# Kernel tuning notes

Measured on AMD Instinct MI355X. Metric: run time of the kernel, lower is better.

The kernel has to match this reference:

```python
import jax, jax.numpy as jnp
import numpy as np

B, S, H, E, TOPK = 4, 2048, 2048, 8, 2


def setup_inputs() -> dict:
    key = jax.random.key(0)
    ks = jax.random.split(key, 3)
    scale_g = 1.0 / np.sqrt(H)
    scale_e = 1.0 / np.sqrt(H)
    return {
        "x": jax.random.normal(ks[0], (B, S, H), dtype=jnp.float32),
        "Wg": jax.random.normal(ks[1], (H, E), dtype=jnp.float32) * scale_g,
        "bg": jnp.zeros((E,), dtype=jnp.float32),
        "We": jax.random.normal(ks[2], (E, H, H), dtype=jnp.float32) * scale_e,
        "be": jnp.zeros((E, H), dtype=jnp.float32),
        "top_k": TOPK,
    }


def reference(x, Wg, bg, We, be, top_k):
    # x: [B, S, H]
    b, s, h = x.shape
    e = Wg.shape[1]
    tok = x.reshape(-1, h)                      # [T, H]
    logits = tok @ Wg + bg                      # [T, E]
    scores = jax.nn.softmax(logits, axis=-1)    # [T, E]
    _, idx = jax.lax.top_k(scores, top_k)       # [T, top_k]
    # per-expert membership mask: token routed to expert iff expert in its top-k
    mask = (idx[:, :, None] == jnp.arange(e)[None, None, :]).any(axis=1)  # [T, E]
    out = jnp.zeros_like(tok)
    for eid in range(e):  # small fixed expert loop (structurally distinct weights)
        gate = jnp.where(mask[:, eid], scores[:, eid], 0.0)  # [T]
        # dense per-expert layer; tokens not routed contribute exactly zero,
        # matching the torch gather -> dense -> scatter-add combine
        out = out + gate[:, None] * (tok @ We[eid] + be[eid])
    return out.reshape(b, s, h)
```

## Files before the change

### kernel.cpp

```cpp
#include <hip/hip_runtime.h>
#include <hip/hip_bf16.h>

#define TOK 8192
#define HD 2048
#define NE 8
#define KTOP 2
#define NSLOT (TOK * KTOP)
#define NCHUNK (TOK / 256)

typedef __attribute__((ext_vector_type(8))) short bf16x8;
typedef __attribute__((ext_vector_type(4))) float f32x4;

#define GLDS16(g, l) __builtin_amdgcn_global_load_lds( \
    (const __attribute__((address_space(1))) void*)(g), \
    (__attribute__((address_space(3))) void*)(l), 16, 0, 0)

__device__ __forceinline__ unsigned short f2bf(float f) {
  union { float f; unsigned u; } v; v.f = f;
  unsigned r = v.u + 0x7fffu + ((v.u >> 16) & 1u);
  return (unsigned short)(r >> 16);
}
__device__ __forceinline__ float bf2f(unsigned short b) {
  union { unsigned u; float f; } v; v.u = ((unsigned)b) << 16;
  return v.f;
}

__global__ __launch_bounds__(256) void routex_kernel(
    const float* __restrict__ x, const float* __restrict__ Wg, const float* __restrict__ bg,
    int* __restrict__ eidx2, float* __restrict__ gate2,
    unsigned short* __restrict__ xbf) {
  __shared__ float xs[HD];
  __shared__ float red[4][NE];
  int t = blockIdx.x;
  int tid = threadIdx.x;
  const float4* xr = (const float4*)(x + (size_t)t * HD);
  float4 a = xr[tid * 2], b = xr[tid * 2 + 1];
  union { bf16x8 v; unsigned short s[8]; } o;
  o.s[0] = f2bf(a.x); o.s[1] = f2bf(a.y); o.s[2] = f2bf(a.z); o.s[3] = f2bf(a.w);
  o.s[4] = f2bf(b.x); o.s[5] = f2bf(b.y); o.s[6] = f2bf(b.z); o.s[7] = f2bf(b.w);
  *(bf16x8*)(xbf + (size_t)t * HD + tid * 8) = o.v;
  *(float4*)(xs + tid * 8) = a;
  *(float4*)(xs + tid * 8 + 4) = b;
  __syncthreads();

  float acc[NE];
#pragma unroll
  for (int e = 0; e < NE; e++) acc[e] = 0.f;
#pragma unroll
  for (int i = 0; i < HD / 256; i++) {
    int k = tid + i * 256;
    float v = xs[k];
    const float4* wr = (const float4*)(Wg + (size_t)k * NE);
    float4 w0 = wr[0], w1 = wr[1];
    acc[0] += v * w0.x; acc[1] += v * w0.y; acc[2] += v * w0.z; acc[3] += v * w0.w;
    acc[4] += v * w1.x; acc[5] += v * w1.y; acc[6] += v * w1.z; acc[7] += v * w1.w;
  }
#pragma unroll
  for (int e = 0; e < NE; e++) {
    float v = acc[e];
#pragma unroll
    for (int s = 32; s > 0; s >>= 1) v += __shfl_xor(v, s, 64);
    acc[e] = v;
  }
  int lane = tid & 63, w = tid >> 6;
  if (lane == 0)
#pragma unroll
    for (int e = 0; e < NE; e++) red[w][e] = acc[e];
  __syncthreads();
  if (tid == 0) {
    float lg[NE];
#pragma unroll
    for (int e = 0; e < NE; e++)
      lg[e] = red[0][e] + red[1][e] + red[2][e] + red[3][e] + bg[e];
    float m = lg[0];
#pragma unroll
    for (int e = 1; e < NE; e++) m = fmaxf(m, lg[e]);
    float p[NE], d = 0.f;
#pragma unroll
    for (int e = 0; e < NE; e++) { p[e] = __expf(lg[e] - m); d += p[e]; }
    float inv = 1.f / d;
    int b0 = 0;
#pragma unroll
    for (int e = 1; e < NE; e++) if (lg[e] > lg[b0]) b0 = e;
    int b1 = (b0 == 0) ? 1 : 0;
#pragma unroll
    for (int e = 0; e < NE; e++) if (e != b0 && lg[e] > lg[b1]) b1 = e;
    eidx2[t * 2 + 0] = b0; gate2[t * 2 + 0] = p[b0] * inv;
    eidx2[t * 2 + 1] = b1; gate2[t * 2 + 1] = p[b1] * inv;
  }
}

__global__ __launch_bounds__(256) void hist_kernel(const int* __restrict__ eidx2,
                                                   int* __restrict__ hist) {
  __shared__ int h[4][NE];
  int b = blockIdx.x, tid = threadIdx.x;
  int lane = tid & 63, w = tid >> 6;
  int t = b * 256 + tid;
  int e0 = eidx2[t * 2], e1 = eidx2[t * 2 + 1];
#pragma unroll
  for (int ee = 0; ee < NE; ee++) {
    unsigned long long m0 = __ballot(e0 == ee);
    unsigned long long m1 = __ballot(e1 == ee);
    if (lane == 0) h[w][ee] = __popcll(m0) + __popcll(m1);
  }
  __syncthreads();
  if (tid < NE) hist[b * NE + tid] = h[0][tid] + h[1][tid] + h[2][tid] + h[3][tid];
}

__global__ void scan_kernel(const int* __restrict__ hist, int* __restrict__ cnt,
                            int* __restrict__ chunk_base) {
  __shared__ int run[NE];
  __shared__ int off[NE];
  __shared__ int cb[NCHUNK][NE];
  int tid = threadIdx.x;
  if (tid < NE) {
    int s = 0;
    for (int b = 0; b < NCHUNK; b++) { cb[b][tid] = s; s += hist[b * NE + tid]; }
    run[tid] = s;
    cnt[tid] = s;
  }
  __syncthreads();
  if (tid == 0) {
    int s = 0;
    for (int e = 0; e < NE; e++) { off[e] = s; s += run[e]; }
  }
  __syncthreads();
  for (int i = tid; i < NCHUNK * NE; i += 64) {
    int b = i / NE, e = i % NE;
    chunk_base[i] = cb[b][e] + off[e];
  }
}

__global__ __launch_bounds__(256) void assign_kernel(
    const int* __restrict__ eidx2, const float* __restrict__ gate2,
    const int* __restrict__ chunk_base,
    int* __restrict__ slot_tok, float* __restrict__ slot_gate, int* __restrict__ tok_slot) {
  __shared__ int wcnt[2][4][NE];
  __shared__ int cbase[NE];
  int b = blockIdx.x;
  int tid = threadIdx.x;
  int lane = tid & 63, w = tid >> 6;
  if (tid < NE) cbase[tid] = chunk_base[b * NE + tid];
  int t = b * 256 + tid;
  int e0 = eidx2[t * 2], e1 = eidx2[t * 2 + 1];
  unsigned long long lt = (1ull << lane) - 1ull;
  int r0 = 0, r1 = 0;
#pragma unroll
  for (int ee = 0; ee < NE; ee++) {
    unsigned long long m0 = __ballot(e0 == ee);
    unsigned long long m1 = __ballot(e1 == ee);
    if (e0 == ee) r0 = __popcll(m0 & lt);
    if (e1 == ee) r1 = __popcll(m1 & lt);
    if (lane == 0) { wcnt[0][w][ee] = __popcll(m0); wcnt[1][w][ee] = __popcll(m1); }
  }
  __syncthreads();
  int base0 = 0, base1 = 0;
#pragma unroll
  for (int p = 0; p < 8; p++) {
    int c0 = wcnt[p >> 2][p & 3][e0];
    int c1 = wcnt[p >> 2][p & 3][e1];
    if (p < w) base0 += c0;
    if (p < 4 + w) base1 += c1;
  }
  int s0 = cbase[e0] + base0 + r0;
  int s1 = cbase[e1] + base1 + r1;
  slot_tok[s0] = t; slot_gate[s0] = gate2[t * 2 + 0];
  slot_tok[s1] = t; slot_gate[s1] = gate2[t * 2 + 1];
  tok_slot[t * 2 + 0] = s0;
  tok_slot[t * 2 + 1] = s1;
}

__global__ __launch_bounds__(256) void wconv_kernel(const float* __restrict__ We,
                                                    unsigned short* __restrict__ Wt) {
  __shared__ float tile[64][65];
  int e = blockIdx.z;
  int k0 = blockIdx.x * 64, n0 = blockIdx.y * 64;
  int t = threadIdx.x;
  const float* src = We + ((size_t)e * HD + k0) * HD + n0;
#pragma unroll
  for (int i = 0; i < 4; i++) {
    int f = t + i * 256;
    int r = f >> 4, c4 = (f & 15) * 4;
    float4 v = *(const float4*)(src + (size_t)r * HD + c4);
    tile[r][c4 + 0] = v.x; tile[r][c4 + 1] = v.y;
    tile[r][c4 + 2] = v.z; tile[r][c4 + 3] = v.w;
  }
  __syncthreads();
  unsigned short* dst = Wt + ((size_t)e * HD + n0) * HD + k0;
#pragma unroll
  for (int i = 0; i < 2; i++) {
    int s = t + i * 256;
    int n = s >> 3, k8 = (s & 7) * 8;
    union { bf16x8 v; unsigned short us[8]; } o;
#pragma unroll
    for (int j = 0; j < 8; j++) o.us[j] = f2bf(tile[k8 + j][n]);
    *(bf16x8*)(dst + (size_t)n * HD + k8) = o.v;
  }
}

#define BM 128
#define BN 128
#define BK 32
#define EPS 72

__global__ __launch_bounds__(256) void moe_gemm(
    const unsigned short* __restrict__ xbf, const unsigned short* __restrict__ Wt,
    const int* __restrict__ cnt, const int* __restrict__ slot_tok,
    const float* __restrict__ be, unsigned short* __restrict__ Ybf) {
  int bid = blockIdx.x;
  int e = bid >> 10;
  int rem = bid & 1023;
  int mt = rem >> 4, nt = rem & 15;
  int off = 0, c = 0;
#pragma unroll
  for (int i = 0; i < NE; i++) { int ci = cnt[i]; if (i < e) off += ci; if (i == e) c = ci; }
  if (mt * BM >= c) return;
  int row0 = off + mt * BM;
  int n0 = nt * BN;

  __shared__ unsigned short Sm[BM * BK + BN * BK];
  unsigned short* As = Sm;
  unsigned short* Bs = Sm + BM * BK;

  int tid = threadIdx.x;
  int lane = tid & 63, w = tid >> 6;
  int wm = w & 1, wn = w >> 1;
  int quad = lane >> 4, l16 = lane & 15;

  int srow = lane >> 2;
  int sq   = lane & 3;
  int ra0 = w * 32 + srow, ra1 = ra0 + 16;
  int sl0 = min(row0 + ra0, NSLOT - 1);
  int sl1 = min(row0 + ra1, NSLOT - 1);
  size_t ta0 = (size_t)slot_tok[sl0], ta1 = (size_t)slot_tok[sl1];
  const unsigned short* gA0 = xbf + ta0 * HD + sq * 8;
  const unsigned short* gA1 = xbf + ta1 * HD + sq * 8;
  const unsigned short* gB0 = Wt + ((size_t)e * HD + n0 + ra0) * HD + sq * 8;
  const unsigned short* gB1 = Wt + ((size_t)e * HD + n0 + ra1) * HD + sq * 8;
  unsigned short* lA0 = As + (w * 32) * BK;
  unsigned short* lA1 = As + (w * 32 + 16) * BK;
  unsigned short* lB0 = Bs + (w * 32) * BK;
  unsigned short* lB1 = Bs + (w * 32 + 16) * BK;

  const unsigned short* pa = As + (wm * 64 + l16) * BK + quad * 8;
  const unsigned short* pb = Bs + (wn * 64 + l16) * BK + quad * 8;

  f32x4 acc[4][4] = {};

  for (int k0 = 0; k0 < HD; k0 += BK) {
    GLDS16(gA0, lA0);
    GLDS16(gA1, lA1);
    GLDS16(gB0, lB0);
    GLDS16(gB1, lB1);
    gA0 += BK; gA1 += BK; gB0 += BK; gB1 += BK;
    __syncthreads();
    bf16x8 af[4], bfr[4];
#pragma unroll
    for (int i = 0; i < 4; i++) {
      af[i]  = *(const bf16x8*)(pa + i * 16 * BK);
      bfr[i] = *(const bf16x8*)(pb + i * 16 * BK);
    }
#pragma unroll
    for (int im = 0; im < 4; im++)
#pragma unroll
      for (int in = 0; in < 4; in++)
        acc[im][in] = __builtin_amdgcn_mfma_f32_16x16x32_bf16(af[im], bfr[in], acc[im][in], 0, 0, 0);
    __syncthreads();
  }

  float bias[4];
#pragma unroll
  for (int in = 0; in < 4; in++)
    bias[in] = be[e * HD + n0 + wn * 64 + in * 16 + l16];

  unsigned short* reg = Sm + w * (16 * EPS);
  int rrow = lane >> 2;
  int rcol = (lane & 3) * 16;
#pragma unroll
  for (int im = 0; im < 4; im++) {
#pragma unroll
    for (int in = 0; in < 4; in++)
#pragma unroll
      for (int r = 0; r < 4; r++)
        reg[(quad * 4 + r) * EPS + in * 16 + l16] = f2bf(acc[im][in][r] + bias[in]);
    __syncthreads();
    int gr = mt * BM + wm * 64 + im * 16 + rrow;
    if (gr < c) {
      bf16x8 v0 = *(const bf16x8*)(reg + rrow * EPS + rcol);
      bf16x8 v1 = *(const bf16x8*)(reg + rrow * EPS + rcol + 8);
      unsigned short* dst = Ybf + (size_t)(off + gr) * HD + n0 + wn * 64 + rcol;
      *(bf16x8*)dst = v0;
      *(bf16x8*)(dst + 8) = v1;
    }
    __syncthreads();
  }
}

__global__ __launch_bounds__(256) void combine_kernel(
    const unsigned short* __restrict__ Ybf, const int* __restrict__ tok_slot,
    const float* __restrict__ slot_gate, float* __restrict__ out) {
  int c8 = threadIdx.x * 8;
#pragma unroll
  for (int i = 0; i < 4; i++) {
    int t = blockIdx.x * 4 + i;
    int s0 = tok_slot[t * 2], s1 = tok_slot[t * 2 + 1];
    float g0 = slot_gate[s0], g1 = slot_gate[s1];
    union { bf16x8 v; unsigned short s[8]; } y0, y1;
    y0.v = *(const bf16x8*)(Ybf + (size_t)s0 * HD + c8);
    y1.v = *(const bf16x8*)(Ybf + (size_t)s1 * HD + c8);
    float4 o0, o1;
    o0.x = g0 * bf2f(y0.s[0]) + g1 * bf2f(y1.s[0]);
    o0.y = g0 * bf2f(y0.s[1]) + g1 * bf2f(y1.s[1]);
    o0.z = g0 * bf2f(y0.s[2]) + g1 * bf2f(y1.s[2]);
    o0.w = g0 * bf2f(y0.s[3]) + g1 * bf2f(y1.s[3]);
    o1.x = g0 * bf2f(y0.s[4]) + g1 * bf2f(y1.s[4]);
    o1.y = g0 * bf2f(y0.s[5]) + g1 * bf2f(y1.s[5]);
    o1.z = g0 * bf2f(y0.s[6]) + g1 * bf2f(y1.s[6]);
    o1.w = g0 * bf2f(y0.s[7]) + g1 * bf2f(y1.s[7]);
    float4* dst = (float4*)(out + (size_t)t * HD + c8);
    dst[0] = o0;
    dst[1] = o1;
  }
}

extern "C" void kernel_launch(void* const* d_in, const int* in_sizes, int n_in,
                              void* d_out, int out_size, void* d_ws, size_t ws_size,
                              hipStream_t stream) {
  const float* x  = (const float*)d_in[0];
  const float* Wg = (const float*)d_in[1];
  const float* bg = (const float*)d_in[2];
  const float* We = (const float*)d_in[3];
  const float* be = (const float*)d_in[4];
  float* out = (float*)d_out;

  char* ws = (char*)d_ws;
  int* cnt        = (int*)ws;
  int* hist       = (int*)(ws + 256);
  int* chunk_base = (int*)(ws + 256 + 1024);
  int* eidx2       = (int*)(ws + 4096);
  float* gate2     = (float*)(ws + 4096 + NSLOT * 4);
  int* slot_tok    = (int*)(ws + 4096 + 2 * NSLOT * 4);
  float* slot_gate = (float*)(ws + 4096 + 3 * NSLOT * 4);
  int* tok_slot    = (int*)(ws + 4096 + 4 * NSLOT * 4);
  unsigned short* xbf = (unsigned short*)(ws + 8192 + 5 * NSLOT * 4);
  unsigned short* Wt  = xbf + (size_t)TOK * HD;
  unsigned short* Ybf = Wt + (size_t)NE * HD * HD;

  routex_kernel<<<TOK, 256, 0, stream>>>(x, Wg, bg, eidx2, gate2, xbf);
  hist_kernel<<<NCHUNK, 256, 0, stream>>>(eidx2, hist);
  scan_kernel<<<1, 64, 0, stream>>>(hist, cnt, chunk_base);
  assign_kernel<<<NCHUNK, 256, 0, stream>>>(eidx2, gate2, chunk_base, slot_tok, slot_gate, tok_slot);
  wconv_kernel<<<dim3(HD / 64, HD / 64, NE), 256, 0, stream>>>(We, Wt);
  moe_gemm<<<NE * 64 * 16, 256, 0, stream>>>(xbf, Wt, cnt, slot_tok, be, Ybf);
  combine_kernel<<<TOK / 4, 256, 0, stream>>>(Ybf, tok_slot, slot_gate, out);
}
```

Baseline: 471.3 us.

## Fuse routing with weight conversion, fold scan into assign, double-buffer GEMM LDS

Interleaves the routing/x-conversion blocks with the weight transpose-to-bf16 blocks in one launch, which removes a kernel boundary and lets the two memory-bound phases overlap. Folds the single-block scan into assign_kernel, where each block recomputes the prefix sums itself. Double-buffers the moe_gemm LDS tiles so the next K-slice load is issued before the current MFMA work, at the cost of twice the shared memory and possibly lower occupancy.

```diff
diff --git a/kernel.cpp b/kernel.cpp
--- a/kernel.cpp
+++ b/kernel.cpp
@@ -25,22 +25,55 @@
   return v.f;
 }
 
-__global__ __launch_bounds__(256) void routex_kernel(
+__global__ __launch_bounds__(256) void route_wconv_kernel(
     const float* __restrict__ x, const float* __restrict__ Wg, const float* __restrict__ bg,
+    const float* __restrict__ We,
     int* __restrict__ eidx2, float* __restrict__ gate2,
-    unsigned short* __restrict__ xbf) {
-  __shared__ float xs[HD];
-  __shared__ float red[4][NE];
-  int t = blockIdx.x;
+    unsigned short* __restrict__ xbf, unsigned short* __restrict__ Wt) {
+  __shared__ union {
+    struct { float xs[HD]; float red[4][NE]; } r;
+    float tile[64][65];
+  } sm;
+  int bid = blockIdx.x;
   int tid = threadIdx.x;
+
+  if (bid & 1) {
+    int i = bid >> 1;
+    int e = i >> 10;
+    int rem = i & 1023;
+    int k0 = (rem >> 5) * 64, n0 = (rem & 31) * 64;
+    const float* src = We + ((size_t)e * HD + k0) * HD + n0;
+#pragma unroll
+    for (int it = 0; it < 4; it++) {
+      int f = tid + it * 256;
+      int r = f >> 4, c4 = (f & 15) * 4;
+      float4 v = *(const float4*)(src + (size_t)r * HD + c4);
+      sm.tile[r][c4 + 0] = v.x; sm.tile[r][c4 + 1] = v.y;
+      sm.tile[r][c4 + 2] = v.z; sm.tile[r][c4 + 3] = v.w;
+    }
+    __syncthreads();
+    unsigned short* dst = Wt + ((size_t)e * HD + n0) * HD + k0;
+#pragma unroll
+    for (int it = 0; it < 2; it++) {
+      int s = tid + it * 256;
+      int n = s >> 3, k8 = (s & 7) * 8;
+      union { bf16x8 v; unsigned short us[8]; } o;
+#pragma unroll
+      for (int j = 0; j < 8; j++) o.us[j] = f2bf(sm.tile[k8 + j][n]);
+      *(bf16x8*)(dst + (size_t)n * HD + k8) = o.v;
+    }
+    return;
+  }
+
+  int t = bid >> 1;
   const float4* xr = (const float4*)(x + (size_t)t * HD);
   float4 a = xr[tid * 2], b = xr[tid * 2 + 1];
   union { bf16x8 v; unsigned short s[8]; } o;
   o.s[0] = f2bf(a.x); o.s[1] = f2bf(a.y); o.s[2] = f2bf(a.z); o.s[3] = f2bf(a.w);
   o.s[4] = f2bf(b.x); o.s[5] = f2bf(b.y); o.s[6] = f2bf(b.z); o.s[7] = f2bf(b.w);
   *(bf16x8*)(xbf + (size_t)t * HD + tid * 8) = o.v;
-  *(float4*)(xs + tid * 8) = a;
-  *(float4*)(xs + tid * 8 + 4) = b;
+  *(float4*)(sm.r.xs + tid * 8) = a;
+  *(float4*)(sm.r.xs + tid * 8 + 4) = b;
   __syncthreads();
 
   float acc[NE];
@@ -49,7 +82,7 @@
 #pragma unroll
   for (int i = 0; i < HD / 256; i++) {
     int k = tid + i * 256;
-    float v = xs[k];
+    float v = sm.r.xs[k];
     const float4* wr = (const float4*)(Wg + (size_t)k * NE);
     float4 w0 = wr[0], w1 = wr[1];
     acc[0] += v * w0.x; acc[1] += v * w0.y; acc[2] += v * w0.z; acc[3] += v * w0.w;
@@ -65,13 +98,13 @@
   int lane = tid & 63, w = tid >> 6;
   if (lane == 0)
 #pragma unroll
-    for (int e = 0; e < NE; e++) red[w][e] = acc[e];
+    for (int e = 0; e < NE; e++) sm.r.red[w][e] = acc[e];
   __syncthreads();
   if (tid == 0) {
     float lg[NE];
 #pragma unroll
     for (int e = 0; e < NE; e++)
-      lg[e] = red[0][e] + red[1][e] + red[2][e] + red[3][e] + bg[e];
+      lg[e] = sm.r.red[0][e] + sm.r.red[1][e] + sm.r.red[2][e] + sm.r.red[3][e] + bg[e];
     float m = lg[0];
 #pragma unroll
     for (int e = 1; e < NE; e++) m = fmaxf(m, lg[e]);
@@ -107,40 +140,24 @@
   if (tid < NE) hist[b * NE + tid] = h[0][tid] + h[1][tid] + h[2][tid] + h[3][tid];
 }
 
-__global__ void scan_kernel(const int* __restrict__ hist, int* __restrict__ cnt,
-                            int* __restrict__ chunk_base) {
-  __shared__ int run[NE];
-  __shared__ int off[NE];
-  __shared__ int cb[NCHUNK][NE];
-  int tid = threadIdx.x;
-  if (tid < NE) {
-    int s = 0;
-    for (int b = 0; b < NCHUNK; b++) { cb[b][tid] = s; s += hist[b * NE + tid]; }
-    run[tid] = s;
-    cnt[tid] = s;
-  }
-  __syncthreads();
-  if (tid == 0) {
-    int s = 0;
-    for (int e = 0; e < NE; e++) { off[e] = s; s += run[e]; }
-  }
-  __syncthreads();
-  for (int i = tid; i < NCHUNK * NE; i += 64) {
-    int b = i / NE, e = i % NE;
-    chunk_base[i] = cb[b][e] + off[e];
-  }
-}
-
 __global__ __launch_bounds__(256) void assign_kernel(
     const int* __restrict__ eidx2, const float* __restrict__ gate2,
-    const int* __restrict__ chunk_base,
+    const int* __restrict__ hist, int* __restrict__ cnt,
     int* __restrict__ slot_tok, float* __restrict__ slot_gate, int* __restrict__ tok_slot) {
   __shared__ int wcnt[2][4][NE];
-  __shared__ int cbase[NE];
+  __shared__ int tot[NE], cbs[NE], cb[NE];
   int b = blockIdx.x;
   int tid = threadIdx.x;
   int lane = tid & 63, w = tid >> 6;
-  if (tid < NE) cbase[tid] = chunk_base[b * NE + tid];
+  if (tid < NE) {
+    int s = 0, base = 0;
+    for (int bb = 0; bb < NCHUNK; bb++) {
+      if (bb == b) base = s;
+      s += hist[bb * NE + tid];
+    }
+    tot[tid] = s; cbs[tid] = base;
+    if (b == 0) cnt[tid] = s;
+  }
   int t = b * 256 + tid;
   int e0 = eidx2[t * 2], e1 = eidx2[t * 2 + 1];
   unsigned long long lt = (1ull << lane) - 1ull;
@@ -154,6 +171,12 @@
     if (lane == 0) { wcnt[0][w][ee] = __popcll(m0); wcnt[1][w][ee] = __popcll(m1); }
   }
   __syncthreads();
+  if (tid == 0) {
+    int o = 0;
+#pragma unroll
+    for (int e = 0; e < NE; e++) { cb[e] = cbs[e] + o; o += tot[e]; }
+  }
+  __syncthreads();
   int base0 = 0, base1 = 0;
 #pragma unroll
   for (int p = 0; p < 8; p++) {
@@ -162,40 +185,12 @@
     if (p < w) base0 += c0;
     if (p < 4 + w) base1 += c1;
   }
-  int s0 = cbase[e0] + base0 + r0;
-  int s1 = cbase[e1] + base1 + r1;
+  int s0 = cb[e0] + base0 + r0;
+  int s1 = cb[e1] + base1 + r1;
   slot_tok[s0] = t; slot_gate[s0] = gate2[t * 2 + 0];
   slot_tok[s1] = t; slot_gate[s1] = gate2[t * 2 + 1];
   tok_slot[t * 2 + 0] = s0;
   tok_slot[t * 2 + 1] = s1;
-}
-
-__global__ __launch_bounds__(256) void wconv_kernel(const float* __restrict__ We,
-                                                    unsigned short* __restrict__ Wt) {
-  __shared__ float tile[64][65];
-  int e = blockIdx.z;
-  int k0 = blockIdx.x * 64, n0 = blockIdx.y * 64;
-  int t = threadIdx.x;
-  const float* src = We + ((size_t)e * HD + k0) * HD + n0;
-#pragma unroll
-  for (int i = 0; i < 4; i++) {
-    int f = t + i * 256;
-    int r = f >> 4, c4 = (f & 15) * 4;
-    float4 v = *(const float4*)(src + (size_t)r * HD + c4);
-    tile[r][c4 + 0] = v.x; tile[r][c4 + 1] = v.y;
-    tile[r][c4 + 2] = v.z; tile[r][c4 + 3] = v.w;
-  }
-  __syncthreads();
-  unsigned short* dst = Wt + ((size_t)e * HD + n0) * HD + k0;
-#pragma unroll
-  for (int i = 0; i < 2; i++) {
-    int s = t + i * 256;
-    int n = s >> 3, k8 = (s & 7) * 8;
-    union { bf16x8 v; unsigned short us[8]; } o;
-#pragma unroll
-    for (int j = 0; j < 8; j++) o.us[j] = f2bf(tile[k8 + j][n]);
-    *(bf16x8*)(dst + (size_t)n * HD + k8) = o.v;
-  }
 }
 
 #define BM 128
@@ -218,9 +213,7 @@
   int row0 = off + mt * BM;
   int n0 = nt * BN;
 
-  __shared__ unsigned short Sm[BM * BK + BN * BK];
-  unsigned short* As = Sm;
-  unsigned short* Bs = Sm + BM * BK;
+  __shared__ unsigned short Sm[2][BM * BK + BN * BK];
 
   int tid = threadIdx.x;
   int lane = tid & 63, w = tid >> 6;
@@ -237,28 +230,39 @@
   const unsigned short* gA1 = xbf + ta1 * HD + sq * 8;
   const unsigned short* gB0 = Wt + ((size_t)e * HD + n0 + ra0) * HD + sq * 8;
   const unsigned short* gB1 = Wt + ((size_t)e * HD + n0 + ra1) * HD + sq * 8;
-  unsigned short* lA0 = As + (w * 32) * BK;
-  unsigned short* lA1 = As + (w * 32 + 16) * BK;
-  unsigned short* lB0 = Bs + (w * 32) * BK;
-  unsigned short* lB1 = Bs + (w * 32 + 16) * BK;
-
-  const unsigned short* pa = As + (wm * 64 + l16) * BK + quad * 8;
-  const unsigned short* pb = Bs + (wn * 64 + l16) * BK + quad * 8;
+  int oA0 = (w * 32) * BK;
+  int oA1 = (w * 32 + 16) * BK;
+  int oB0 = BM * BK + (w * 32) * BK;
+  int oB1 = BM * BK + (w * 32 + 16) * BK;
+
+  int pa_off = (wm * 64 + l16) * BK + quad * 8;
+  int pb_off = BM * BK + (wn * 64 + l16) * BK + quad * 8;
 
   f32x4 acc[4][4] = {};
 
-  for (int k0 = 0; k0 < HD; k0 += BK) {
-    GLDS16(gA0, lA0);
-    GLDS16(gA1, lA1);
-    GLDS16(gB0, lB0);
-    GLDS16(gB1, lB1);
-    gA0 += BK; gA1 += BK; gB0 += BK; gB1 += BK;
-    __syncthreads();
+  GLDS16(gA0, &Sm[0][oA0]);
+  GLDS16(gA1, &Sm[0][oA1]);
+  GLDS16(gB0, &Sm[0][oB0]);
+  GLDS16(gB1, &Sm[0][oB1]);
+  gA0 += BK; gA1 += BK; gB0 += BK; gB1 += BK;
+  __syncthreads();
+
+  int cur = 0;
+  for (int kt = 0; kt < HD / BK; ++kt) {
+    if (kt + 1 < HD / BK) {
+      unsigned short* nb = Sm[cur ^ 1];
+      GLDS16(gA0, nb + oA0);
+      GLDS16(gA1, nb + oA1);
+      GLDS16(gB0, nb + oB0);
+      GLDS16(gB1, nb + oB1);
+      gA0 += BK; gA1 += BK; gB0 += BK; gB1 += BK;
+    }
+    const unsigned short* base = Sm[cur];
     bf16x8 af[4], bfr[4];
 #pragma unroll
     for (int i = 0; i < 4; i++) {
-      af[i]  = *(const bf16x8*)(pa + i * 16 * BK);
-      bfr[i] = *(const bf16x8*)(pb + i * 16 * BK);
+      af[i]  = *(const bf16x8*)(base + pa_off + i * 16 * BK);
+      bfr[i] = *(const bf16x8*)(base + pb_off + i * 16 * BK);
     }
 #pragma unroll
     for (int im = 0; im < 4; im++)
@@ -266,6 +270,7 @@
       for (int in = 0; in < 4; in++)
         acc[im][in] = __builtin_amdgcn_mfma_f32_16x16x32_bf16(af[im], bfr[in], acc[im][in], 0, 0, 0);
     __syncthreads();
+    cur ^= 1;
   }
 
   float bias[4];
@@ -273,7 +278,7 @@
   for (int in = 0; in < 4; in++)
     bias[in] = be[e * HD + n0 + wn * 64 + in * 16 + l16];
 
-  unsigned short* reg = Sm + w * (16 * EPS);
+  unsigned short* reg = &Sm[0][0] + w * (16 * EPS);
   int rrow = lane >> 2;
   int rcol = (lane & 3) * 16;
 #pragma unroll
@@ -336,7 +341,6 @@
   char* ws = (char*)d_ws;
   int* cnt        = (int*)ws;
   int* hist       = (int*)(ws + 256);
-  int* chunk_base = (int*)(ws + 256 + 1024);
   int* eidx2       = (int*)(ws + 4096);
   float* gate2     = (float*)(ws + 4096 + NSLOT * 4);
   int* slot_tok    = (int*)(ws + 4096 + 2 * NSLOT * 4);
@@ -346,11 +350,9 @@
   unsigned short* Wt  = xbf + (size_t)TOK * HD;
   unsigned short* Ybf = Wt + (size_t)NE * HD * HD;
 
-  routex_kernel<<<TOK, 256, 0, stream>>>(x, Wg, bg, eidx2, gate2, xbf);
+  route_wconv_kernel<<<2 * TOK, 256, 0, stream>>>(x, Wg, bg, We, eidx2, gate2, xbf, Wt);
   hist_kernel<<<NCHUNK, 256, 0, stream>>>(eidx2, hist);
-  scan_kernel<<<1, 64, 0, stream>>>(hist, cnt, chunk_base);
-  assign_kernel<<<NCHUNK, 256, 0, stream>>>(eidx2, gate2, chunk_base, slot_tok, slot_gate, tok_slot);
-  wconv_kernel<<<dim3(HD / 64, HD / 64, NE), 256, 0, stream>>>(We, Wt);
+  assign_kernel<<<NCHUNK, 256, 0, stream>>>(eidx2, gate2, hist, cnt, slot_tok, slot_gate, tok_slot);
   moe_gemm<<<NE * 64 * 16, 256, 0, stream>>>(xbf, Wt, cnt, slot_tok, be, Ybf);
   combine_kernel<<<TOK / 4, 256, 0, stream>>>(Ybf, tok_slot, slot_gate, out);
 }
```

Result: slower. 489.3 us (+3.8%).
